# Performance work log

Measured on AMD Instinct MI355X. Metric: run time of the kernel, lower is better.

Reference implementation:

```python
import jax, jax.numpy as jnp
import numpy as np

DIM = 512
HEADS = 8
DIM_HEAD = 32
INNER = HEADS * DIM_HEAD  # 256
B, N = 2, 2048
EPS = 1e-5


def setup_inputs() -> dict:
    key = jax.random.key(0)
    ks = jax.random.split(key, 6)
    x = jax.random.normal(ks[0], (B, N, DIM), dtype=jnp.float32)
    rel_pos_bias = jax.random.normal(ks[1], (HEADS, N, N), dtype=jnp.float32)
    ln_scale = jnp.ones((DIM,), dtype=jnp.float32)
    w_qkv = jax.random.normal(ks[2], (DIM, INNER * 3), dtype=jnp.float32) / np.sqrt(DIM)
    w_out = jax.random.normal(ks[3], (INNER, DIM), dtype=jnp.float32) / np.sqrt(INNER)
    b_out = jnp.zeros((DIM,), dtype=jnp.float32)
    return {"x": x, "rel_pos_bias": rel_pos_bias, "ln_scale": ln_scale,
            "w_qkv": w_qkv, "w_out": w_out, "b_out": b_out}


def reference(x, rel_pos_bias, ln_scale, w_qkv, w_out, b_out):
    scale = DIM_HEAD ** -0.5
    # LayerNorm (no bias), eps=1e-5
    mu = jnp.mean(x, axis=-1, keepdims=True)
    var = jnp.mean(jnp.square(x - mu), axis=-1, keepdims=True)
    xn = (x - mu) * jax.lax.rsqrt(var + EPS) * ln_scale
    # fused QKV projection, no bias
    qkv = xn @ w_qkv  # [b, n, 3*inner]
    q, k, v = jnp.split(qkv, 3, axis=-1)
    def to_heads(t):
        b, n, _ = t.shape
        return t.reshape(b, n, HEADS, DIM_HEAD).transpose(0, 2, 1, 3)  # b h n d
    q, k, v = map(to_heads, (q, k, v))
    q = q * scale
    sim = jnp.einsum('bhid,bhjd->bhij', q, k)
    sim = sim + rel_pos_bias  # (h,n,n) broadcasts over batch
    attn = jax.nn.softmax(sim, axis=-1)
    o = jnp.einsum('bhij,bhjd->bhid', attn, v)
    o = o.transpose(0, 2, 1, 3).reshape(x.shape[0], x.shape[1], INNER)  # b n (h d)
    return o @ w_out + b_out
```

## Files before the change

kernel.cpp:

```cpp
#include <hip/hip_runtime.h>
#include <hip/hip_bf16.h>
#include <cstdint>

#define NB 2
#define NSEQ 2048
#define NDIM 512
#define NHEAD 8
#define DHEAD 32
#define NINNER 256
#define NQKV 768
#define LNEPS 1e-5f
#define QSCALE 0.17677669529663687f

typedef short short8 __attribute__((ext_vector_type(8)));
typedef float f32x4 __attribute__((ext_vector_type(4)));
typedef unsigned int u32x4 __attribute__((ext_vector_type(4)));
typedef unsigned int u32x2 __attribute__((ext_vector_type(2)));
typedef unsigned short u16;
typedef unsigned int u32;

__device__ __forceinline__ f32x4 mfma16(short8 a, short8 b, f32x4 c) {
    return __builtin_amdgcn_mfma_f32_16x16x32_bf16(a, b, c, 0, 0, 0);
}

__device__ __forceinline__ u16 f2bf(float a) {
    union { float f; u32 u; } x; x.f = a;
    u32 r = x.u + 0x7fffu + ((x.u >> 16) & 1u);
    return (u16)(r >> 16);
}
__device__ __forceinline__ float bf2f(u16 h) {
    union { float f; u32 u; } x; x.u = ((u32)h) << 16; return x.f;
}
__device__ __forceinline__ void split2(float a, u16& hi, u16& lo) {
    hi = f2bf(a);
    lo = f2bf(a - bf2f(hi));
}
__device__ __forceinline__ u32 pk2(float a, float b) {
    return (u32)f2bf(a) | ((u32)f2bf(b) << 16);
}

__global__ __launch_bounds__(256) void ln_kernel(
    const float* __restrict__ x, const float* __restrict__ gamma,
    u32* __restrict__ xn_hi, u32* __restrict__ xn_lo)
{
    const int row = blockIdx.x;
    const int t = threadIdx.x;
    const float2 v = ((const float2*)(x + (size_t)row * NDIM))[t];
    float s1 = v.x + v.y;
    float s2 = v.x * v.x + v.y * v.y;
    #pragma unroll
    for (int off = 32; off >= 1; off >>= 1) {
        s1 += __shfl_down(s1, off);
        s2 += __shfl_down(s2, off);
    }
    __shared__ float a1[4], a2[4];
    if ((t & 63) == 0) { a1[t >> 6] = s1; a2[t >> 6] = s2; }
    __syncthreads();
    const float ts1 = a1[0] + a1[1] + a1[2] + a1[3];
    const float ts2 = a2[0] + a2[1] + a2[2] + a2[3];
    const float mu = ts1 * (1.0f / NDIM);
    const float var = ts2 * (1.0f / NDIM) - mu * mu;
    const float rs = rsqrtf(var + LNEPS);
    const float2 g = ((const float2*)gamma)[t];
    u16 h0, l0, h1, l1;
    split2((v.x - mu) * rs * g.x, h0, l0);
    split2((v.y - mu) * rs * g.y, h1, l1);
    xn_hi[(size_t)row * (NDIM / 2) + t] = (u32)h0 | ((u32)h1 << 16);
    xn_lo[(size_t)row * (NDIM / 2) + t] = (u32)l0 | ((u32)l1 << 16);
}

__global__ __launch_bounds__(256) void wtrans_kernel(
    const float* __restrict__ w, u16* __restrict__ wT_hi, u16* __restrict__ wT_lo,
    int K, int N)
{
    __shared__ __align__(16) u16 th[64][72], tl[64][72];
    const int t = threadIdx.x;
    const int k0 = blockIdx.x * 64, n0 = blockIdx.y * 64;
    {
        const int k = t >> 2, c = (t & 3) * 16;
        const float* src = w + (size_t)(k0 + k) * N + n0 + c;
        #pragma unroll
        for (int jj = 0; jj < 4; jj++) {
            const f32x4 w4 = *(const f32x4*)(src + jj * 4);
            #pragma unroll
            for (int e = 0; e < 4; e++) {
                u16 hh, ll;
                split2(w4[e], hh, ll);
                th[k][c + jj * 4 + e] = hh;
                tl[k][c + jj * 4 + e] = ll;
            }
        }
    }
    __syncthreads();
    {
        const int n = t >> 2, kc = (t & 3) * 16;
        u16 hb[16], lb[16];
        #pragma unroll
        for (int j = 0; j < 16; j++) { hb[j] = th[kc + j][n]; lb[j] = tl[kc + j][n]; }
        u16* dh = wT_hi + (size_t)(n0 + n) * K + k0 + kc;
        u16* dl = wT_lo + (size_t)(n0 + n) * K + k0 + kc;
        *(short8*)dh = *(short8*)hb;
        *(short8*)(dh + 8) = *(short8*)(hb + 8);
        *(short8*)dl = *(short8*)lb;
        *(short8*)(dl + 8) = *(short8*)(lb + 8);
    }
}

__global__ __launch_bounds__(256) void vtrans_kernel(
    const u16* __restrict__ v, u16* __restrict__ vt)
{
    __shared__ __align__(16) u16 sh[64][40];
    const int t = threadIdx.x;
    const int n0 = blockIdx.x * 64;
    const int bh = blockIdx.y;
    {
        const int n = t >> 2, c = (t & 3) * 8;
        *(short8*)&sh[n][c] = *(const short8*)(v + ((size_t)bh * NSEQ + n0 + n) * DHEAD + c);
    }
    __syncthreads();
    {
        const int d = t >> 3, nc = (t & 7) * 8;
        u16 buf[8];
        #pragma unroll
        for (int j = 0; j < 8; j++) buf[j] = sh[nc + j][d];
        *(short8*)(vt + ((size_t)bh * DHEAD + d) * NSEQ + n0 + nc) = *(short8*)buf;
    }
}

__global__ __launch_bounds__(256, 4) void qkv_kernel(
    const u16* __restrict__ xn_hi, const u16* __restrict__ xn_lo,
    const u16* __restrict__ wT_hi, const u16* __restrict__ wT_lo,
    u16* __restrict__ q_hi, u16* __restrict__ q_lo,
    u16* __restrict__ k_hi, u16* __restrict__ k_lo,
    u16* __restrict__ v)
{
    __shared__ __align__(16) u16 Ah[32][40], Al[32][40], Bh[64][40], Bl[64][40];
    const int t = threadIdx.x;
    const int wave = t >> 6, lane = t & 63;
    const int lrow = lane & 15, lquad = lane >> 4;
    const int rowBase = blockIdx.x * 32;
    const int colBase = blockIdx.y * 64;
    const int wm = (wave & 1) * 16;
    const int wn = (wave >> 1) * 32;
    const int kf = lquad * 8;
    const f32x4 zero = {0.f, 0.f, 0.f, 0.f};
    f32x4 acc0 = zero, acc1 = zero;

    const int tar = (t & 127) >> 2, tac = ((t & 127) & 3) * 8;
    const int tbr = t >> 2, tbc = (t & 3) * 8;

    for (int k0 = 0; k0 < NDIM; k0 += 32) {
        __syncthreads();
        if (t < 128)
            *(short8*)&Ah[tar][tac] = *(const short8*)(xn_hi + (size_t)(rowBase + tar) * NDIM + k0 + tac);
        else
            *(short8*)&Al[tar][tac] = *(const short8*)(xn_lo + (size_t)(rowBase + tar) * NDIM + k0 + tac);
        *(short8*)&Bh[tbr][tbc] = *(const short8*)(wT_hi + (size_t)(colBase + tbr) * NDIM + k0 + tbc);
        *(short8*)&Bl[tbr][tbc] = *(const short8*)(wT_lo + (size_t)(colBase + tbr) * NDIM + k0 + tbc);
        __syncthreads();
        const short8 ah = *(const short8*)&Ah[wm + lrow][kf];
        const short8 al = *(const short8*)&Al[wm + lrow][kf];
        const short8 b0h = *(const short8*)&Bh[wn + lrow][kf];
        const short8 b0l = *(const short8*)&Bl[wn + lrow][kf];
        const short8 b1h = *(const short8*)&Bh[wn + 16 + lrow][kf];
        const short8 b1l = *(const short8*)&Bl[wn + 16 + lrow][kf];
        acc0 = mfma16(ah, b0h, acc0); acc0 = mfma16(ah, b0l, acc0); acc0 = mfma16(al, b0h, acc0);
        acc1 = mfma16(ah, b1h, acc1); acc1 = mfma16(ah, b1l, acc1); acc1 = mfma16(al, b1h, acc1);
    }

    #pragma unroll
    for (int ni = 0; ni < 2; ni++) {
        const f32x4 acc = ni ? acc1 : acc0;
        #pragma unroll
        for (int r = 0; r < 4; r++) {
            const int grow = rowBase + wm + lquad * 4 + r;
            const int gcol = colBase + wn + ni * 16 + lrow;
            const float val = acc[r];
            const int bidx = grow >> 11;
            const int n = grow & (NSEQ - 1);
            const int sec = gcol >> 8;
            const int idx = gcol & 255;
            const int head = idx >> 5, d = idx & 31;
            const int bh = bidx * NHEAD + head;
            if (sec == 0) {
                u16 hh, ll;
                split2(val * QSCALE, hh, ll);
                const size_t a = ((size_t)bh * NSEQ + n) * DHEAD + d;
                q_hi[a] = hh; q_lo[a] = ll;
            } else if (sec == 1) {
                u16 hh, ll;
                split2(val, hh, ll);
                const size_t a = ((size_t)bh * NSEQ + n) * DHEAD + d;
                k_hi[a] = hh; k_lo[a] = ll;
            } else {
                v[((size_t)bh * NSEQ + n) * DHEAD + d] = f2bf(val);
            }
        }
    }
}

__global__ __launch_bounds__(256, 4) void attn_kernel(
    const u16* __restrict__ q_hi, const u16* __restrict__ q_lo,
    const u16* __restrict__ k_hi, const u16* __restrict__ k_lo,
    const u16* __restrict__ vt,
    const float* __restrict__ bias,
    u16* __restrict__ o_hi, u16* __restrict__ o_lo)
{
    __shared__ __align__(16) float cA[2][4][64][4];
    __shared__ __align__(16) float cB[2][4][64][4];
    __shared__ float cl[2][4][16];
    const int t = threadIdx.x;
    const int wave = t >> 6, lane = t & 63;
    const int lrow = lane & 15, lquad = lane >> 4;
    const int head = blockIdx.y;
    const int qb = blockIdx.x * 16;
    const size_t qk0 = (size_t)head * NSEQ * DHEAD;
    const size_t qk1 = (size_t)(NHEAD + head) * NSEQ * DHEAD;
    const size_t qoff = (size_t)(qb + lrow) * DHEAD + lquad * 8;
    const short8 qh0 = *(const short8*)(q_hi + qk0 + qoff);
    const short8 ql0 = *(const short8*)(q_lo + qk0 + qoff);
    const short8 qh1 = *(const short8*)(q_hi + qk1 + qoff);
    const short8 ql1 = *(const short8*)(q_lo + qk1 + qoff);
    const f32x4 zero = {0.f, 0.f, 0.f, 0.f};
    f32x4 accA0 = zero, accB0 = zero, accA1 = zero, accB1 = zero;
    float lp0 = 0.f, lp1 = 0.f;
    const float* bptr = bias + (size_t)head * NSEQ * NSEQ + (size_t)(qb + lrow) * NSEQ;
    const int kt0 = wave * 512;
    const int src1 = lrow | (((2 * lquad) & 3) << 4);
    const int src2 = lrow | (((2 * lquad + 1) & 3) << 4);
    const bool qtop = lquad < 2;

    for (int i = 0; i < 16; i++) {
        const int kt = kt0 + i * 32;
        const size_t koff = (size_t)(kt + lrow) * DHEAD + lquad * 8;
        const short8 ka0h = *(const short8*)(k_hi + qk0 + koff);
        const short8 ka0l = *(const short8*)(k_lo + qk0 + koff);
        const short8 ka1h = *(const short8*)(k_hi + qk0 + koff + 16 * DHEAD);
        const short8 ka1l = *(const short8*)(k_lo + qk0 + koff + 16 * DHEAD);
        const short8 kb0h = *(const short8*)(k_hi + qk1 + koff);
        const short8 kb0l = *(const short8*)(k_lo + qk1 + koff);
        const short8 kb1h = *(const short8*)(k_hi + qk1 + koff + 16 * DHEAD);
        const short8 kb1l = *(const short8*)(k_lo + qk1 + koff + 16 * DHEAD);
        const short8 va0 = *(const short8*)(vt + qk0 + (size_t)lrow * NSEQ + kt + lquad * 8);
        const short8 va1 = *(const short8*)(vt + qk0 + (size_t)(16 + lrow) * NSEQ + kt + lquad * 8);
        const short8 vb0 = *(const short8*)(vt + qk1 + (size_t)lrow * NSEQ + kt + lquad * 8);
        const short8 vb1 = *(const short8*)(vt + qk1 + (size_t)(16 + lrow) * NSEQ + kt + lquad * 8);
        const f32x4 bias0 = *(const f32x4*)(bptr + kt + lquad * 4);
        const f32x4 bias1 = *(const f32x4*)(bptr + kt + 16 + lquad * 4);

        {
            f32x4 c0 = zero, c1 = zero;
            c0 = mfma16(ka0h, qh0, c0); c0 = mfma16(ka0h, ql0, c0); c0 = mfma16(ka0l, qh0, c0);
            c1 = mfma16(ka1h, qh0, c1); c1 = mfma16(ka1h, ql0, c1); c1 = mfma16(ka1l, qh0, c1);
            f32x4 p0, p1;
            #pragma unroll
            for (int r = 0; r < 4; r++) {
                p0[r] = __expf(c0[r] + bias0[r]);
                p1[r] = __expf(c1[r] + bias1[r]);
            }
            lp0 += (p0[0] + p0[1]) + (p0[2] + p0[3]) + (p1[0] + p1[1]) + (p1[2] + p1[3]);
            const u32 a0 = pk2(p0[0], p0[1]), a1 = pk2(p0[2], p0[3]);
            const u32 b0 = pk2(p1[0], p1[1]), b1 = pk2(p1[2], p1[3]);
            const u32 s1a0 = (u32)__shfl((int)a0, src1), s1a1 = (u32)__shfl((int)a1, src1);
            const u32 s1b0 = (u32)__shfl((int)b0, src1), s1b1 = (u32)__shfl((int)b1, src1);
            const u32 s2a0 = (u32)__shfl((int)a0, src2), s2a1 = (u32)__shfl((int)a1, src2);
            const u32 s2b0 = (u32)__shfl((int)b0, src2), s2b1 = (u32)__shfl((int)b1, src2);
            union { u32x4 u; short8 s; } cv;
            cv.u[0] = qtop ? s1a0 : s1b0;
            cv.u[1] = qtop ? s1a1 : s1b1;
            cv.u[2] = qtop ? s2a0 : s2b0;
            cv.u[3] = qtop ? s2a1 : s2b1;
            accA0 = mfma16(va0, cv.s, accA0);
            accB0 = mfma16(va1, cv.s, accB0);
        }
        {
            f32x4 c0 = zero, c1 = zero;
            c0 = mfma16(kb0h, qh1, c0); c0 = mfma16(kb0h, ql1, c0); c0 = mfma16(kb0l, qh1, c0);
            c1 = mfma16(kb1h, qh1, c1); c1 = mfma16(kb1h, ql1, c1); c1 = mfma16(kb1l, qh1, c1);
            f32x4 p0, p1;
            #pragma unroll
            for (int r = 0; r < 4; r++) {
                p0[r] = __expf(c0[r] + bias0[r]);
                p1[r] = __expf(c1[r] + bias1[r]);
            }
            lp1 += (p0[0] + p0[1]) + (p0[2] + p0[3]) + (p1[0] + p1[1]) + (p1[2] + p1[3]);
            const u32 a0 = pk2(p0[0], p0[1]), a1 = pk2(p0[2], p0[3]);
            const u32 b0 = pk2(p1[0], p1[1]), b1 = pk2(p1[2], p1[3]);
            const u32 s1a0 = (u32)__shfl((int)a0, src1), s1a1 = (u32)__shfl((int)a1, src1);
            const u32 s1b0 = (u32)__shfl((int)b0, src1), s1b1 = (u32)__shfl((int)b1, src1);
            const u32 s2a0 = (u32)__shfl((int)a0, src2), s2a1 = (u32)__shfl((int)a1, src2);
            const u32 s2b0 = (u32)__shfl((int)b0, src2), s2b1 = (u32)__shfl((int)b1, src2);
            union { u32x4 u; short8 s; } cv;
            cv.u[0] = qtop ? s1a0 : s1b0;
            cv.u[1] = qtop ? s1a1 : s1b1;
            cv.u[2] = qtop ? s2a0 : s2b0;
            cv.u[3] = qtop ? s2a1 : s2b1;
            accA1 = mfma16(vb0, cv.s, accA1);
            accB1 = mfma16(vb1, cv.s, accB1);
        }
    }

    lp0 += __shfl_xor(lp0, 16); lp0 += __shfl_xor(lp0, 32);
    lp1 += __shfl_xor(lp1, 16); lp1 += __shfl_xor(lp1, 32);

    *(f32x4*)&cA[0][wave][lane][0] = accA0;
    *(f32x4*)&cB[0][wave][lane][0] = accB0;
    *(f32x4*)&cA[1][wave][lane][0] = accA1;
    *(f32x4*)&cB[1][wave][lane][0] = accB1;
    if (lquad == 0) {
        cl[0][wave][lrow] = lp0;
        cl[1][wave][lrow] = lp1;
    }
    __syncthreads();
    if (wave < 2) {
        const int b = wave;
        f32x4 sA = *(const f32x4*)&cA[b][0][lane][0];
        f32x4 sB = *(const f32x4*)&cB[b][0][lane][0];
        #pragma unroll
        for (int w = 1; w < 4; w++) {
            sA += *(const f32x4*)&cA[b][w][lane][0];
            sB += *(const f32x4*)&cB[b][w][lane][0];
        }
        const float lt = cl[b][0][lrow] + cl[b][1][lrow] + cl[b][2][lrow] + cl[b][3][lrow];
        const float inv = 1.0f / lt;
        const size_t base = ((size_t)b * NSEQ + qb + lrow) * NINNER + head * DHEAD + lquad * 4;
        u16 h[8], l[8];
        #pragma unroll
        for (int r = 0; r < 4; r++) {
            split2(sA[r] * inv, h[r], l[r]);
            split2(sB[r] * inv, h[4 + r], l[4 + r]);
        }
        *(u32x2*)&o_hi[base] = *(u32x2*)&h[0];
        *(u32x2*)&o_hi[base + 16] = *(u32x2*)&h[4];
        *(u32x2*)&o_lo[base] = *(u32x2*)&l[0];
        *(u32x2*)&o_lo[base + 16] = *(u32x2*)&l[4];
    }
}

__global__ __launch_bounds__(256, 4) void out_kernel(
    const u16* __restrict__ o_hi, const u16* __restrict__ o_lo,
    const u16* __restrict__ wT_hi, const u16* __restrict__ wT_lo,
    const float* __restrict__ b_out,
    float* __restrict__ out)
{
    __shared__ __align__(16) u16 Ah[32][40], Al[32][40], Bh[64][40], Bl[64][40];
    const int t = threadIdx.x;
    const int wave = t >> 6, lane = t & 63;
    const int lrow = lane & 15, lquad = lane >> 4;
    const int rowBase = blockIdx.x * 32;
    const int colBase = blockIdx.y * 64;
    const int wm = (wave & 1) * 16;
    const int wn = (wave >> 1) * 32;
    const int kf = lquad * 8;
    const f32x4 zero = {0.f, 0.f, 0.f, 0.f};
    f32x4 acc0 = zero, acc1 = zero;

    const int tar = (t & 127) >> 2, tac = ((t & 127) & 3) * 8;
    const int tbr = t >> 2, tbc = (t & 3) * 8;

    for (int k0 = 0; k0 < NINNER; k0 += 32) {
        __syncthreads();
        if (t < 128)
            *(short8*)&Ah[tar][tac] = *(const short8*)(o_hi + (size_t)(rowBase + tar) * NINNER + k0 + tac);
        else
            *(short8*)&Al[tar][tac] = *(const short8*)(o_lo + (size_t)(rowBase + tar) * NINNER + k0 + tac);
        *(short8*)&Bh[tbr][tbc] = *(const short8*)(wT_hi + (size_t)(colBase + tbr) * NINNER + k0 + tbc);
        *(short8*)&Bl[tbr][tbc] = *(const short8*)(wT_lo + (size_t)(colBase + tbr) * NINNER + k0 + tbc);
        __syncthreads();
        const short8 ah = *(const short8*)&Ah[wm + lrow][kf];
        const short8 al = *(const short8*)&Al[wm + lrow][kf];
        const short8 b0h = *(const short8*)&Bh[wn + lrow][kf];
        const short8 b0l = *(const short8*)&Bl[wn + lrow][kf];
        const short8 b1h = *(const short8*)&Bh[wn + 16 + lrow][kf];
        const short8 b1l = *(const short8*)&Bl[wn + 16 + lrow][kf];
        acc0 = mfma16(ah, b0h, acc0); acc0 = mfma16(ah, b0l, acc0); acc0 = mfma16(al, b0h, acc0);
        acc1 = mfma16(ah, b1h, acc1); acc1 = mfma16(ah, b1l, acc1); acc1 = mfma16(al, b1h, acc1);
    }

    #pragma unroll
    for (int ni = 0; ni < 2; ni++) {
        const f32x4 acc = ni ? acc1 : acc0;
        #pragma unroll
        for (int r = 0; r < 4; r++) {
            const int grow = rowBase + wm + lquad * 4 + r;
            const int gcol = colBase + wn + ni * 16 + lrow;
            out[(size_t)grow * NDIM + gcol] = acc[r] + b_out[gcol];
        }
    }
}

extern "C" void kernel_launch(void* const* d_in, const int* in_sizes, int n_in,
                              void* d_out, int out_size, void* d_ws, size_t ws_size,
                              hipStream_t stream)
{
    (void)in_sizes; (void)n_in; (void)out_size; (void)ws_size;
    const float* x     = (const float*)d_in[0];
    const float* bias  = (const float*)d_in[1];
    const float* gamma = (const float*)d_in[2];
    const float* wqkv  = (const float*)d_in[3];
    const float* wout  = (const float*)d_in[4];
    const float* bout  = (const float*)d_in[5];
    float* out = (float*)d_out;

    char* ws = (char*)d_ws;
    size_t off = 0;
    auto carve = [&](size_t bytes) -> void* {
        void* p = (void*)(ws + off);
        off += (bytes + 255) & ~(size_t)255;
        return p;
    };
    const size_t rows = (size_t)NB * NSEQ;
    const size_t hn = (size_t)NB * NHEAD * NSEQ * DHEAD;
    u16* xn_hi = (u16*)carve(rows * NDIM * 2);
    u16* xn_lo = (u16*)carve(rows * NDIM * 2);
    u16* wqT_hi = (u16*)carve((size_t)NQKV * NDIM * 2);
    u16* wqT_lo = (u16*)carve((size_t)NQKV * NDIM * 2);
    u16* woT_hi = (u16*)carve((size_t)NDIM * NINNER * 2);
    u16* woT_lo = (u16*)carve((size_t)NDIM * NINNER * 2);
    u16* q_hi  = (u16*)carve(hn * 2);
    u16* q_lo  = (u16*)carve(hn * 2);
    u16* k_hi  = (u16*)carve(hn * 2);
    u16* k_lo  = (u16*)carve(hn * 2);
    u16* vbuf  = (u16*)carve(hn * 2);
    u16* vt    = (u16*)carve(hn * 2);
    u16* o_hi  = (u16*)carve(rows * NINNER * 2);
    u16* o_lo  = (u16*)carve(rows * NINNER * 2);

    ln_kernel<<<dim3((unsigned)rows), 256, 0, stream>>>(x, gamma, (u32*)xn_hi, (u32*)xn_lo);
    wtrans_kernel<<<dim3(NDIM / 64, NQKV / 64), 256, 0, stream>>>(wqkv, wqT_hi, wqT_lo, NDIM, NQKV);
    wtrans_kernel<<<dim3(NINNER / 64, NDIM / 64), 256, 0, stream>>>(wout, woT_hi, woT_lo, NINNER, NDIM);
    qkv_kernel<<<dim3(128, 12), 256, 0, stream>>>(xn_hi, xn_lo, wqT_hi, wqT_lo,
                                                  q_hi, q_lo, k_hi, k_lo, vbuf);
    vtrans_kernel<<<dim3(NSEQ / 64, NB * NHEAD), 256, 0, stream>>>(vbuf, vt);
    attn_kernel<<<dim3(128, 8), 256, 0, stream>>>(q_hi, q_lo, k_hi, k_lo,
                                                  vt, bias, o_hi, o_lo);
    out_kernel<<<dim3(128, 8), 256, 0, stream>>>(o_hi, o_lo, woT_hi, woT_lo, bout, out);
}
```

Before: 308.6 us.

## Split attention batches across waves, enlarge GEMM tiles, merge weight transposes

The attention kernel moves from 256 to 512 threads, so each wave handles one batch and one key slice instead of both batches. A permuted key row order lets the P fragment feed the PV MFMA directly, removing the cross-lane shuffles. The QKV and output GEMMs grow to 64x64 tiles with a 2x2 MFMA tile per wave, which improves operand reuse and halves the grid. The two weight-transpose launches are merged into one. Risks are higher register pressure at 512 threads and fewer blocks in flight for the GEMMs.

Measured after the change: 308.5 us. About the same (-0.0%).

```diff
diff --git a/kernel.cpp b/kernel.cpp
--- a/kernel.cpp
+++ b/kernel.cpp
@@ -70,12 +70,20 @@
 }
 
 __global__ __launch_bounds__(256) void wtrans_kernel(
-    const float* __restrict__ w, u16* __restrict__ wT_hi, u16* __restrict__ wT_lo,
-    int K, int N)
+    const float* __restrict__ wq, u16* __restrict__ wqT_hi, u16* __restrict__ wqT_lo,
+    const float* __restrict__ wo, u16* __restrict__ woT_hi, u16* __restrict__ woT_lo)
 {
     __shared__ __align__(16) u16 th[64][72], tl[64][72];
     const int t = threadIdx.x;
-    const int k0 = blockIdx.x * 64, n0 = blockIdx.y * 64;
+    const float* w; u16 *wT_hi, *wT_lo; int K, N, k0, n0;
+    if (blockIdx.x < 96) {
+        w = wq; wT_hi = wqT_hi; wT_lo = wqT_lo; K = NDIM; N = NQKV;
+        k0 = (blockIdx.x & 7) * 64; n0 = (blockIdx.x >> 3) * 64;
+    } else {
+        const int b = blockIdx.x - 96;
+        w = wo; wT_hi = woT_hi; wT_lo = woT_lo; K = NINNER; N = NDIM;
+        k0 = (b & 3) * 64; n0 = (b >> 2) * 64;
+    }
     {
         const int k = t >> 2, c = (t & 3) * 16;
         const float* src = w + (size_t)(k0 + k) * N + n0 + c;
@@ -134,72 +142,76 @@
     u16* __restrict__ k_hi, u16* __restrict__ k_lo,
     u16* __restrict__ v)
 {
-    __shared__ __align__(16) u16 Ah[32][40], Al[32][40], Bh[64][40], Bl[64][40];
+    __shared__ __align__(16) u16 Ah[64][40], Al[64][40], Bh[64][40], Bl[64][40];
     const int t = threadIdx.x;
     const int wave = t >> 6, lane = t & 63;
     const int lrow = lane & 15, lquad = lane >> 4;
-    const int rowBase = blockIdx.x * 32;
+    const int rowBase = blockIdx.x * 64;
     const int colBase = blockIdx.y * 64;
-    const int wm = (wave & 1) * 16;
+    const int wm = (wave & 1) * 32;
     const int wn = (wave >> 1) * 32;
     const int kf = lquad * 8;
     const f32x4 zero = {0.f, 0.f, 0.f, 0.f};
-    f32x4 acc0 = zero, acc1 = zero;
-
-    const int tar = (t & 127) >> 2, tac = ((t & 127) & 3) * 8;
-    const int tbr = t >> 2, tbc = (t & 3) * 8;
+    f32x4 acc[2][2];
+    acc[0][0] = zero; acc[0][1] = zero; acc[1][0] = zero; acc[1][1] = zero;
+
+    const int sr = t >> 2, sc = (t & 3) * 8;
 
     for (int k0 = 0; k0 < NDIM; k0 += 32) {
         __syncthreads();
-        if (t < 128)
-            *(short8*)&Ah[tar][tac] = *(const short8*)(xn_hi + (size_t)(rowBase + tar) * NDIM + k0 + tac);
-        else
-            *(short8*)&Al[tar][tac] = *(const short8*)(xn_lo + (size_t)(rowBase + tar) * NDIM + k0 + tac);
-        *(short8*)&Bh[tbr][tbc] = *(const short8*)(wT_hi + (size_t)(colBase + tbr) * NDIM + k0 + tbc);
-        *(short8*)&Bl[tbr][tbc] = *(const short8*)(wT_lo + (size_t)(colBase + tbr) * NDIM + k0 + tbc);
+        *(short8*)&Ah[sr][sc] = *(const short8*)(xn_hi + (size_t)(rowBase + sr) * NDIM + k0 + sc);
+        *(short8*)&Al[sr][sc] = *(const short8*)(xn_lo + (size_t)(rowBase + sr) * NDIM + k0 + sc);
+        *(short8*)&Bh[sr][sc] = *(const short8*)(wT_hi + (size_t)(colBase + sr) * NDIM + k0 + sc);
+        *(short8*)&Bl[sr][sc] = *(const short8*)(wT_lo + (size_t)(colBase + sr) * NDIM + k0 + sc);
         __syncthreads();
-        const short8 ah = *(const short8*)&Ah[wm + lrow][kf];
-        const short8 al = *(const short8*)&Al[wm + lrow][kf];
+        const short8 a0h = *(const short8*)&Ah[wm + lrow][kf];
+        const short8 a0l = *(const short8*)&Al[wm + lrow][kf];
+        const short8 a1h = *(const short8*)&Ah[wm + 16 + lrow][kf];
+        const short8 a1l = *(const short8*)&Al[wm + 16 + lrow][kf];
         const short8 b0h = *(const short8*)&Bh[wn + lrow][kf];
         const short8 b0l = *(const short8*)&Bl[wn + lrow][kf];
         const short8 b1h = *(const short8*)&Bh[wn + 16 + lrow][kf];
         const short8 b1l = *(const short8*)&Bl[wn + 16 + lrow][kf];
-        acc0 = mfma16(ah, b0h, acc0); acc0 = mfma16(ah, b0l, acc0); acc0 = mfma16(al, b0h, acc0);
-        acc1 = mfma16(ah, b1h, acc1); acc1 = mfma16(ah, b1l, acc1); acc1 = mfma16(al, b1h, acc1);
+        acc[0][0] = mfma16(a0h, b0h, acc[0][0]); acc[0][0] = mfma16(a0h, b0l, acc[0][0]); acc[0][0] = mfma16(a0l, b0h, acc[0][0]);
+        acc[0][1] = mfma16(a0h, b1h, acc[0][1]); acc[0][1] = mfma16(a0h, b1l, acc[0][1]); acc[0][1] = mfma16(a0l, b1h, acc[0][1]);
+        acc[1][0] = mfma16(a1h, b0h, acc[1][0]); acc[1][0] = mfma16(a1h, b0l, acc[1][0]); acc[1][0] = mfma16(a1l, b0h, acc[1][0]);
+        acc[1][1] = mfma16(a1h, b1h, acc[1][1]); acc[1][1] = mfma16(a1h, b1l, acc[1][1]); acc[1][1] = mfma16(a1l, b1h, acc[1][1]);
     }
 
     #pragma unroll
-    for (int ni = 0; ni < 2; ni++) {
-        const f32x4 acc = ni ? acc1 : acc0;
-        #pragma unroll
-        for (int r = 0; r < 4; r++) {
-            const int grow = rowBase + wm + lquad * 4 + r;
-            const int gcol = colBase + wn + ni * 16 + lrow;
-            const float val = acc[r];
-            const int bidx = grow >> 11;
-            const int n = grow & (NSEQ - 1);
-            const int sec = gcol >> 8;
-            const int idx = gcol & 255;
-            const int head = idx >> 5, d = idx & 31;
-            const int bh = bidx * NHEAD + head;
-            if (sec == 0) {
-                u16 hh, ll;
-                split2(val * QSCALE, hh, ll);
-                const size_t a = ((size_t)bh * NSEQ + n) * DHEAD + d;
-                q_hi[a] = hh; q_lo[a] = ll;
-            } else if (sec == 1) {
-                u16 hh, ll;
-                split2(val, hh, ll);
-                const size_t a = ((size_t)bh * NSEQ + n) * DHEAD + d;
-                k_hi[a] = hh; k_lo[a] = ll;
-            } else {
-                v[((size_t)bh * NSEQ + n) * DHEAD + d] = f2bf(val);
+    for (int mi = 0; mi < 2; mi++) {
+        #pragma unroll
+        for (int ni = 0; ni < 2; ni++) {
+            #pragma unroll
+            for (int r = 0; r < 4; r++) {
+                const int grow = rowBase + wm + mi * 16 + lquad * 4 + r;
+                const int gcol = colBase + wn + ni * 16 + lrow;
+                const float val = acc[mi][ni][r];
+                const int bidx = grow >> 11;
+                const int n = grow & (NSEQ - 1);
+                const int sec = gcol >> 8;
+                const int idx = gcol & 255;
+                const int head = idx >> 5, d = idx & 31;
+                const int bh = bidx * NHEAD + head;
+                if (sec == 0) {
+                    u16 hh, ll;
+                    split2(val * QSCALE, hh, ll);
+                    const size_t a = ((size_t)bh * NSEQ + n) * DHEAD + d;
+                    q_hi[a] = hh; q_lo[a] = ll;
+                } else if (sec == 1) {
+                    u16 hh, ll;
+                    split2(val, hh, ll);
+                    const size_t a = ((size_t)bh * NSEQ + n) * DHEAD + d;
+                    k_hi[a] = hh; k_lo[a] = ll;
+                } else {
+                    v[((size_t)bh * NSEQ + n) * DHEAD + d] = f2bf(val);
+                }
             }
         }
     }
 }
 
-__global__ __launch_bounds__(256, 4) void attn_kernel(
+__global__ __launch_bounds__(512, 8) void attn_kernel(
     const u16* __restrict__ q_hi, const u16* __restrict__ q_lo,
     const u16* __restrict__ k_hi, const u16* __restrict__ k_lo,
     const u16* __restrict__ vt,
@@ -212,118 +224,70 @@
     const int t = threadIdx.x;
     const int wave = t >> 6, lane = t & 63;
     const int lrow = lane & 15, lquad = lane >> 4;
+    const int batch = wave >> 2, wslice = wave & 3;
     const int head = blockIdx.y;
     const int qb = blockIdx.x * 16;
-    const size_t qk0 = (size_t)head * NSEQ * DHEAD;
-    const size_t qk1 = (size_t)(NHEAD + head) * NSEQ * DHEAD;
+    const size_t qkb = (size_t)(batch * NHEAD + head) * NSEQ * DHEAD;
     const size_t qoff = (size_t)(qb + lrow) * DHEAD + lquad * 8;
-    const short8 qh0 = *(const short8*)(q_hi + qk0 + qoff);
-    const short8 ql0 = *(const short8*)(q_lo + qk0 + qoff);
-    const short8 qh1 = *(const short8*)(q_hi + qk1 + qoff);
-    const short8 ql1 = *(const short8*)(q_lo + qk1 + qoff);
+    const short8 qh = *(const short8*)(q_hi + qkb + qoff);
+    const short8 ql = *(const short8*)(q_lo + qkb + qoff);
     const f32x4 zero = {0.f, 0.f, 0.f, 0.f};
-    f32x4 accA0 = zero, accB0 = zero, accA1 = zero, accB1 = zero;
-    float lp0 = 0.f, lp1 = 0.f;
+    f32x4 accA = zero, accB = zero;
+    float lp = 0.f;
+    const int kperm = ((lrow >> 2) << 3) | (lrow & 3);
     const float* bptr = bias + (size_t)head * NSEQ * NSEQ + (size_t)(qb + lrow) * NSEQ;
-    const int kt0 = wave * 512;
-    const int src1 = lrow | (((2 * lquad) & 3) << 4);
-    const int src2 = lrow | (((2 * lquad + 1) & 3) << 4);
-    const bool qtop = lquad < 2;
+    const int kt0 = wslice * 512;
 
     for (int i = 0; i < 16; i++) {
         const int kt = kt0 + i * 32;
-        const size_t koff = (size_t)(kt + lrow) * DHEAD + lquad * 8;
-        const short8 ka0h = *(const short8*)(k_hi + qk0 + koff);
-        const short8 ka0l = *(const short8*)(k_lo + qk0 + koff);
-        const short8 ka1h = *(const short8*)(k_hi + qk0 + koff + 16 * DHEAD);
-        const short8 ka1l = *(const short8*)(k_lo + qk0 + koff + 16 * DHEAD);
-        const short8 kb0h = *(const short8*)(k_hi + qk1 + koff);
-        const short8 kb0l = *(const short8*)(k_lo + qk1 + koff);
-        const short8 kb1h = *(const short8*)(k_hi + qk1 + koff + 16 * DHEAD);
-        const short8 kb1l = *(const short8*)(k_lo + qk1 + koff + 16 * DHEAD);
-        const short8 va0 = *(const short8*)(vt + qk0 + (size_t)lrow * NSEQ + kt + lquad * 8);
-        const short8 va1 = *(const short8*)(vt + qk0 + (size_t)(16 + lrow) * NSEQ + kt + lquad * 8);
-        const short8 vb0 = *(const short8*)(vt + qk1 + (size_t)lrow * NSEQ + kt + lquad * 8);
-        const short8 vb1 = *(const short8*)(vt + qk1 + (size_t)(16 + lrow) * NSEQ + kt + lquad * 8);
-        const f32x4 bias0 = *(const f32x4*)(bptr + kt + lquad * 4);
-        const f32x4 bias1 = *(const f32x4*)(bptr + kt + 16 + lquad * 4);
-
-        {
-            f32x4 c0 = zero, c1 = zero;
-            c0 = mfma16(ka0h, qh0, c0); c0 = mfma16(ka0h, ql0, c0); c0 = mfma16(ka0l, qh0, c0);
-            c1 = mfma16(ka1h, qh0, c1); c1 = mfma16(ka1h, ql0, c1); c1 = mfma16(ka1l, qh0, c1);
-            f32x4 p0, p1;
-            #pragma unroll
-            for (int r = 0; r < 4; r++) {
-                p0[r] = __expf(c0[r] + bias0[r]);
-                p1[r] = __expf(c1[r] + bias1[r]);
-            }
-            lp0 += (p0[0] + p0[1]) + (p0[2] + p0[3]) + (p1[0] + p1[1]) + (p1[2] + p1[3]);
-            const u32 a0 = pk2(p0[0], p0[1]), a1 = pk2(p0[2], p0[3]);
-            const u32 b0 = pk2(p1[0], p1[1]), b1 = pk2(p1[2], p1[3]);
-            const u32 s1a0 = (u32)__shfl((int)a0, src1), s1a1 = (u32)__shfl((int)a1, src1);
-            const u32 s1b0 = (u32)__shfl((int)b0, src1), s1b1 = (u32)__shfl((int)b1, src1);
-            const u32 s2a0 = (u32)__shfl((int)a0, src2), s2a1 = (u32)__shfl((int)a1, src2);
-            const u32 s2b0 = (u32)__shfl((int)b0, src2), s2b1 = (u32)__shfl((int)b1, src2);
-            union { u32x4 u; short8 s; } cv;
-            cv.u[0] = qtop ? s1a0 : s1b0;
-            cv.u[1] = qtop ? s1a1 : s1b1;
-            cv.u[2] = qtop ? s2a0 : s2b0;
-            cv.u[3] = qtop ? s2a1 : s2b1;
-            accA0 = mfma16(va0, cv.s, accA0);
-            accB0 = mfma16(va1, cv.s, accB0);
-        }
-        {
-            f32x4 c0 = zero, c1 = zero;
-            c0 = mfma16(kb0h, qh1, c0); c0 = mfma16(kb0h, ql1, c0); c0 = mfma16(kb0l, qh1, c0);
-            c1 = mfma16(kb1h, qh1, c1); c1 = mfma16(kb1h, ql1, c1); c1 = mfma16(kb1l, qh1, c1);
-            f32x4 p0, p1;
-            #pragma unroll
-            for (int r = 0; r < 4; r++) {
-                p0[r] = __expf(c0[r] + bias0[r]);
-                p1[r] = __expf(c1[r] + bias1[r]);
-            }
-            lp1 += (p0[0] + p0[1]) + (p0[2] + p0[3]) + (p1[0] + p1[1]) + (p1[2] + p1[3]);
-            const u32 a0 = pk2(p0[0], p0[1]), a1 = pk2(p0[2], p0[3]);
-            const u32 b0 = pk2(p1[0], p1[1]), b1 = pk2(p1[2], p1[3]);
-            const u32 s1a0 = (u32)__shfl((int)a0, src1), s1a1 = (u32)__shfl((int)a1, src1);
-            const u32 s1b0 = (u32)__shfl((int)b0, src1), s1b1 = (u32)__shfl((int)b1, src1);
-            const u32 s2a0 = (u32)__shfl((int)a0, src2), s2a1 = (u32)__shfl((int)a1, src2);
-            const u32 s2b0 = (u32)__shfl((int)b0, src2), s2b1 = (u32)__shfl((int)b1, src2);
-            union { u32x4 u; short8 s; } cv;
-            cv.u[0] = qtop ? s1a0 : s1b0;
-            cv.u[1] = qtop ? s1a1 : s1b1;
-            cv.u[2] = qtop ? s2a0 : s2b0;
-            cv.u[3] = qtop ? s2a1 : s2b1;
-            accA1 = mfma16(vb0, cv.s, accA1);
-            accB1 = mfma16(vb1, cv.s, accB1);
-        }
-    }
-
-    lp0 += __shfl_xor(lp0, 16); lp0 += __shfl_xor(lp0, 32);
-    lp1 += __shfl_xor(lp1, 16); lp1 += __shfl_xor(lp1, 32);
-
-    *(f32x4*)&cA[0][wave][lane][0] = accA0;
-    *(f32x4*)&cB[0][wave][lane][0] = accB0;
-    *(f32x4*)&cA[1][wave][lane][0] = accA1;
-    *(f32x4*)&cB[1][wave][lane][0] = accB1;
-    if (lquad == 0) {
-        cl[0][wave][lrow] = lp0;
-        cl[1][wave][lrow] = lp1;
-    }
+        const size_t kof = (size_t)(kt + kperm) * DHEAD + lquad * 8;
+        const short8 k0h = *(const short8*)(k_hi + qkb + kof);
+        const short8 k0l = *(const short8*)(k_lo + qkb + kof);
+        const short8 k1h = *(const short8*)(k_hi + qkb + kof + 4 * DHEAD);
+        const short8 k1l = *(const short8*)(k_lo + qkb + kof + 4 * DHEAD);
+        const short8 va0 = *(const short8*)(vt + qkb + (size_t)lrow * NSEQ + kt + lquad * 8);
+        const short8 va1 = *(const short8*)(vt + qkb + (size_t)(16 + lrow) * NSEQ + kt + lquad * 8);
+        const f32x4 bias0 = *(const f32x4*)(bptr + kt + lquad * 8);
+        const f32x4 bias1 = *(const f32x4*)(bptr + kt + lquad * 8 + 4);
+
+        f32x4 c0 = zero, c1 = zero;
+        c0 = mfma16(k0h, qh, c0); c0 = mfma16(k0h, ql, c0); c0 = mfma16(k0l, qh, c0);
+        c1 = mfma16(k1h, qh, c1); c1 = mfma16(k1h, ql, c1); c1 = mfma16(k1l, qh, c1);
+        f32x4 p0, p1;
+        #pragma unroll
+        for (int r = 0; r < 4; r++) {
+            p0[r] = __expf(c0[r] + bias0[r]);
+            p1[r] = __expf(c1[r] + bias1[r]);
+        }
+        lp += (p0[0] + p0[1]) + (p0[2] + p0[3]) + (p1[0] + p1[1]) + (p1[2] + p1[3]);
+        union { u32x4 u; short8 s; } cv;
+        cv.u[0] = pk2(p0[0], p0[1]);
+        cv.u[1] = pk2(p0[2], p0[3]);
+        cv.u[2] = pk2(p1[0], p1[1]);
+        cv.u[3] = pk2(p1[2], p1[3]);
+        accA = mfma16(va0, cv.s, accA);
+        accB = mfma16(va1, cv.s, accB);
+    }
+
+    lp += __shfl_xor(lp, 16);
+    lp += __shfl_xor(lp, 32);
+
+    *(f32x4*)&cA[batch][wslice][lane][0] = accA;
+    *(f32x4*)&cB[batch][wslice][lane][0] = accB;
+    if (lquad == 0) cl[batch][wslice][lrow] = lp;
     __syncthreads();
-    if (wave < 2) {
-        const int b = wave;
-        f32x4 sA = *(const f32x4*)&cA[b][0][lane][0];
-        f32x4 sB = *(const f32x4*)&cB[b][0][lane][0];
+    if (wslice == 0) {
+        f32x4 sA = *(const f32x4*)&cA[batch][0][lane][0];
+        f32x4 sB = *(const f32x4*)&cB[batch][0][lane][0];
         #pragma unroll
         for (int w = 1; w < 4; w++) {
-            sA += *(const f32x4*)&cA[b][w][lane][0];
-            sB += *(const f32x4*)&cB[b][w][lane][0];
-        }
-        const float lt = cl[b][0][lrow] + cl[b][1][lrow] + cl[b][2][lrow] + cl[b][3][lrow];
+            sA += *(const f32x4*)&cA[batch][w][lane][0];
+            sB += *(const f32x4*)&cB[batch][w][lane][0];
+        }
+        const float lt = cl[batch][0][lrow] + cl[batch][1][lrow]
+                       + cl[batch][2][lrow] + cl[batch][3][lrow];
         const float inv = 1.0f / lt;
-        const size_t base = ((size_t)b * NSEQ + qb + lrow) * NINNER + head * DHEAD + lquad * 4;
+        const size_t base = ((size_t)batch * NSEQ + qb + lrow) * NINNER + head * DHEAD + lquad * 4;
         u16 h[8], l[8];
         #pragma unroll
         for (int r = 0; r < 4; r++) {
@@ -343,48 +307,52 @@
     const float* __restrict__ b_out,
     float* __restrict__ out)
 {
-    __shared__ __align__(16) u16 Ah[32][40], Al[32][40], Bh[64][40], Bl[64][40];
+    __shared__ __align__(16) u16 Ah[64][40], Al[64][40], Bh[64][40], Bl[64][40];
     const int t = threadIdx.x;
     const int wave = t >> 6, lane = t & 63;
     const int lrow = lane & 15, lquad = lane >> 4;
-    const int rowBase = blockIdx.x * 32;
+    const int rowBase = blockIdx.x * 64;
     const int colBase = blockIdx.y * 64;
-    const int wm = (wave & 1) * 16;
+    const int wm = (wave & 1) * 32;
     const int wn = (wave >> 1) * 32;
     const int kf = lquad * 8;
     const f32x4 zero = {0.f, 0.f, 0.f, 0.f};
-    f32x4 acc0 = zero, acc1 = zero;
-
-    const int tar = (t & 127) >> 2, tac = ((t & 127) & 3) * 8;
-    const int tbr = t >> 2, tbc = (t & 3) * 8;
+    f32x4 acc[2][2];
+    acc[0][0] = zero; acc[0][1] = zero; acc[1][0] = zero; acc[1][1] = zero;
+
+    const int sr = t >> 2, sc = (t & 3) * 8;
 
     for (int k0 = 0; k0 < NINNER; k0 += 32) {
         __syncthreads();
-        if (t < 128)
-            *(short8*)&Ah[tar][tac] = *(const short8*)(o_hi + (size_t)(rowBase + tar) * NINNER + k0 + tac);
-        else
-            *(short8*)&Al[tar][tac] = *(const short8*)(o_lo + (size_t)(rowBase + tar) * NINNER + k0 + tac);
-        *(short8*)&Bh[tbr][tbc] = *(const short8*)(wT_hi + (size_t)(colBase + tbr) * NINNER + k0 + tbc);
-        *(short8*)&Bl[tbr][tbc] = *(const short8*)(wT_lo + (size_t)(colBase + tbr) * NINNER + k0 + tbc);
+        *(short8*)&Ah[sr][sc] = *(const short8*)(o_hi + (size_t)(rowBase + sr) * NINNER + k0 + sc);
+        *(short8*)&Al[sr][sc] = *(const short8*)(o_lo + (size_t)(rowBase + sr) * NINNER + k0 + sc);
+        *(short8*)&Bh[sr][sc] = *(const short8*)(wT_hi + (size_t)(colBase + sr) * NINNER + k0 + sc);
+        *(short8*)&Bl[sr][sc] = *(const short8*)(wT_lo + (size_t)(colBase + sr) * NINNER + k0 + sc);
         __syncthreads();
-        const short8 ah = *(const short8*)&Ah[wm + lrow][kf];
-        const short8 al = *(const short8*)&Al[wm + lrow][kf];
+        const short8 a0h = *(const short8*)&Ah[wm + lrow][kf];
+        const short8 a0l = *(const short8*)&Al[wm + lrow][kf];
+        const short8 a1h = *(const short8*)&Ah[wm + 16 + lrow][kf];
+        const short8 a1l = *(const short8*)&Al[wm + 16 + lrow][kf];
         const short8 b0h = *(const short8*)&Bh[wn + lrow][kf];
         const short8 b0l = *(const short8*)&Bl[wn + lrow][kf];
         const short8 b1h = *(const short8*)&Bh[wn + 16 + lrow][kf];
         const short8 b1l = *(const short8*)&Bl[wn + 16 + lrow][kf];
-        acc0 = mfma16(ah, b0h, acc0); acc0 = mfma16(ah, b0l, acc0); acc0 = mfma16(al, b0h, acc0);
-        acc1 = mfma16(ah, b1h, acc1); acc1 = mfma16(ah, b1l, acc1); acc1 = mfma16(al, b1h, acc1);
+        acc[0][0] = mfma16(a0h, b0h, acc[0][0]); acc[0][0] = mfma16(a0h, b0l, acc[0][0]); acc[0][0] = mfma16(a0l, b0h, acc[0][0]);
+        acc[0][1] = mfma16(a0h, b1h, acc[0][1]); acc[0][1] = mfma16(a0h, b1l, acc[0][1]); acc[0][1] = mfma16(a0l, b1h, acc[0][1]);
+        acc[1][0] = mfma16(a1h, b0h, acc[1][0]); acc[1][0] = mfma16(a1h, b0l, acc[1][0]); acc[1][0] = mfma16(a1l, b0h, acc[1][0]);
+        acc[1][1] = mfma16(a1h, b1h, acc[1][1]); acc[1][1] = mfma16(a1h, b1l, acc[1][1]); acc[1][1] = mfma16(a1l, b1h, acc[1][1]);
     }
 
     #pragma unroll
-    for (int ni = 0; ni < 2; ni++) {
-        const f32x4 acc = ni ? acc1 : acc0;
-        #pragma unroll
-        for (int r = 0; r < 4; r++) {
-            const int grow = rowBase + wm + lquad * 4 + r;
-            const int gcol = colBase + wn + ni * 16 + lrow;
-            out[(size_t)grow * NDIM + gcol] = acc[r] + b_out[gcol];
+    for (int mi = 0; mi < 2; mi++) {
+        #pragma unroll
+        for (int ni = 0; ni < 2; ni++) {
+            #pragma unroll
+            for (int r = 0; r < 4; r++) {
+                const int grow = rowBase + wm + mi * 16 + lquad * 4 + r;
+                const int gcol = colBase + wn + ni * 16 + lrow;
+                out[(size_t)grow * NDIM + gcol] = acc[mi][ni][r] + b_out[gcol];
+            }
         }
     }
 }
@@ -427,12 +395,11 @@
     u16* o_lo  = (u16*)carve(rows * NINNER * 2);
 
     ln_kernel<<<dim3((unsigned)rows), 256, 0, stream>>>(x, gamma, (u32*)xn_hi, (u32*)xn_lo);
-    wtrans_kernel<<<dim3(NDIM / 64, NQKV / 64), 256, 0, stream>>>(wqkv, wqT_hi, wqT_lo, NDIM, NQKV);
-    wtrans_kernel<<<dim3(NINNER / 64, NDIM / 64), 256, 0, stream>>>(wout, woT_hi, woT_lo, NINNER, NDIM);
-    qkv_kernel<<<dim3(128, 12), 256, 0, stream>>>(xn_hi, xn_lo, wqT_hi, wqT_lo,
-                                                  q_hi, q_lo, k_hi, k_lo, vbuf);
+    wtrans_kernel<<<dim3(128), 256, 0, stream>>>(wqkv, wqT_hi, wqT_lo, wout, woT_hi, woT_lo);
+    qkv_kernel<<<dim3(64, 12), 256, 0, stream>>>(xn_hi, xn_lo, wqT_hi, wqT_lo,
+                                                 q_hi, q_lo, k_hi, k_lo, vbuf);
     vtrans_kernel<<<dim3(NSEQ / 64, NB * NHEAD), 256, 0, stream>>>(vbuf, vt);
-    attn_kernel<<<dim3(128, 8), 256, 0, stream>>>(q_hi, q_lo, k_hi, k_lo,
+    attn_kernel<<<dim3(128, 8), 512, 0, stream>>>(q_hi, q_lo, k_hi, k_lo,
                                                   vt, bias, o_hi, o_lo);
-    out_kernel<<<dim3(128, 8), 256, 0, stream>>>(o_hi, o_lo, woT_hi, woT_lo, bout, out);
-}
+    out_kernel<<<dim3(64, 8), 256, 0, stream>>>(o_hi, o_lo, woT_hi, woT_lo, bout, out);
+}
```
